# Kernel tuning notes

Hardware: AMD Instinct MI355X
Metric: run time of the kernel (lower is better)

Reference implementation:

```python
import jax, jax.numpy as jnp
import numpy as np


def _decode(out, anchors, t, case, thresh):
    # out: [B, 3*D, H, W] -> [B, H, W, 3, D]; D = 5 + n_classes
    B, C, H, W = out.shape
    o = jnp.transpose(out, (0, 2, 3, 1)).reshape(B, H, W, 3, C // 3)
    mask = o[..., 0] > thresh  # objectness logit threshold (pre-sigmoid, as in original)
    dt = out.dtype
    gx = jnp.arange(W, dtype=dt)  # grid x runs along W (index[:,2] in original)
    gy = jnp.arange(H, dtype=dt)  # grid y runs along H (index[:,1] in original)
    scale = t / case
    cx = (gx[None, None, :, None] + o[..., 1]) * scale
    cy = (gy[None, :, None, None] + o[..., 2]) * scale
    w = anchors[None, None, None, :, 0] * jnp.exp(o[..., 3]) / case
    h = anchors[None, None, None, :, 1] * jnp.exp(o[..., 4]) / case
    p = jax.nn.sigmoid(o[..., 0])
    cls_idx = jnp.argmax(o[..., 5:], axis=-1).astype(dt)
    boxes = jnp.stack([p, cx, cy, w, h, cls_idx], axis=-1).reshape(-1, 6)
    return boxes, mask.reshape(-1)


def setup_inputs() -> dict:
    key = jax.random.key(0)
    k13, k26, k52, kt = jax.random.split(key, 4)
    B = 32
    inp = {
        "output_13": jax.random.normal(k13, (B, 255, 13, 13), dtype=jnp.float32),
        "output_26": jax.random.normal(k26, (B, 255, 26, 26), dtype=jnp.float32),
        "output_52": jax.random.normal(k52, (B, 255, 52, 52), dtype=jnp.float32),
        # canonical YOLOv3 pixel anchors per scale
        "anchors_13": jnp.array([[116.0, 90.0], [156.0, 198.0], [373.0, 326.0]], dtype=jnp.float32),
        "anchors_26": jnp.array([[30.0, 61.0], [62.0, 45.0], [59.0, 119.0]], dtype=jnp.float32),
        "anchors_52": jnp.array([[10.0, 13.0], [16.0, 30.0], [33.0, 23.0]], dtype=jnp.float32),
        "thresh": jnp.array([0.5], dtype=jnp.float32),
        "case": 416,
    }
    return inp


def reference(output_13, output_26, output_52, anchors_13, anchors_26, anchors_52, thresh, case):
    th = thresh[0]
    b13, m13 = _decode(output_13, anchors_13, 32.0, case, th)
    b26, m26 = _decode(output_26, anchors_26, 16.0, case, th)
    b52, m52 = _decode(output_52, anchors_52, 8.0, case, th)
    boxes = jnp.concatenate([b13, b26, b52], axis=0)  # [N_total, 6], row-major (b,h,w,a) per scale
    mask = jnp.concatenate([m13, m26, m52], axis=0)   # boxes[mask] == original torch.cat output
    return boxes, mask
```

## Files before the change

kernel.cpp:

```cpp
#include <hip/hip_runtime.h>


#define NCLS 80

template<int HW, int W>
__device__ __forceinline__ void decode4(
    const float* __restrict__ in, const float* __restrict__ anch,
    float scale, float inv_case, float th,
    int a, int t, int row_base, int B,
    float* __restrict__ boxes, float* __restrict__ mask)
{
    if (t >= B * HW * 4) return;
    const int rt  = t >> 2;
    const int seg = t & 3;
    const int b   = rt / HW;
    const int hw  = rt - b * HW;

    const float* p = in + ((size_t)b * 255 + (size_t)a * 85) * HW + hw;

    const float* pc = p + (size_t)(5 + seg * 20) * HW;
    float v[20];
#pragma unroll
    for (int j = 0; j < 20; ++j)
        v[j] = pc[(size_t)j * HW];

    float best = v[0];
    int   bi   = seg * 20;
#pragma unroll
    for (int j = 1; j < 20; ++j)
        if (v[j] > best) { best = v[j]; bi = seg * 20 + j; }

    float o0 = p[0 * (size_t)HW];
    float o1 = p[1 * (size_t)HW];
    float o2 = p[2 * (size_t)HW];
    float o3 = p[3 * (size_t)HW];
    float o4 = p[4 * (size_t)HW];

#pragma unroll
    for (int m = 1; m <= 2; m <<= 1) {
        float ob = __shfl_xor(best, m);
        int   oi = __shfl_xor(bi,   m);
        if (ob > best || (ob == best && oi < bi)) { best = ob; bi = oi; }
    }

    if (seg == 0) {
        int h = hw / W;
        int w = hw - h * W;
        float px = 1.0f / (1.0f + __expf(-o0));
        float cx = ((float)w + o1) * scale;
        float cy = ((float)h + o2) * scale;
        float bw = anch[2 * a + 0] * __expf(o3) * inv_case;
        float bh = anch[2 * a + 1] * __expf(o4) * inv_case;

        int row = row_base + rt * 3 + a;
        float2* ob2 = reinterpret_cast<float2*>(boxes + (size_t)row * 6);
        ob2[0] = make_float2(px, cx);
        ob2[1] = make_float2(cy, bw);
        ob2[2] = make_float2(bh, (float)bi);
        mask[row] = (o0 > th) ? 1.0f : 0.0f;
    }
}

__global__ __launch_bounds__(256) void detector_kernel(
    const float* __restrict__ in13, const float* __restrict__ in26,
    const float* __restrict__ in52,
    const float* __restrict__ a13, const float* __restrict__ a26,
    const float* __restrict__ a52,
    const float* __restrict__ thp, const int* __restrict__ casep,
    float* __restrict__ boxes, float* __restrict__ mask,
    int B, int nb52, int nb26)
{
    const int a  = blockIdx.y;
    const int bx = blockIdx.x;
    const float th       = thp[0];
    const float inv_case = 1.0f / (float)casep[0];

    if (bx < nb52) {
        int t = bx * 256 + threadIdx.x;
        decode4<2704, 52>(in52, a52, 8.0f * inv_case, inv_case, th,
                          a, t, B * (169 + 676) * 3, B, boxes, mask);
    } else if (bx < nb52 + nb26) {
        int t = (bx - nb52) * 256 + threadIdx.x;
        decode4<676, 26>(in26, a26, 16.0f * inv_case, inv_case, th,
                         a, t, B * 169 * 3, B, boxes, mask);
    } else {
        int t = (bx - nb52 - nb26) * 256 + threadIdx.x;
        decode4<169, 13>(in13, a13, 32.0f * inv_case, inv_case, th,
                         a, t, 0, B, boxes, mask);
    }
}

extern "C" void kernel_launch(void* const* d_in, const int* in_sizes, int n_in,
                              void* d_out, int out_size, void* d_ws, size_t ws_size,
                              hipStream_t stream) {
    const float* in13 = (const float*)d_in[0];
    const float* in26 = (const float*)d_in[1];
    const float* in52 = (const float*)d_in[2];
    const float* a13  = (const float*)d_in[3];
    const float* a26  = (const float*)d_in[4];
    const float* a52  = (const float*)d_in[5];
    const float* thp  = (const float*)d_in[6];
    const int*   casep = (const int*)d_in[7];

    const int B = in_sizes[0] / (255 * 169);

    const int nb52 = (B * 2704 * 4 + 255) / 256;
    const int nb26 = (B * 676  * 4 + 255) / 256;
    const int nb13 = (B * 169  * 4 + 255) / 256;

    const int nrows = B * (169 + 676 + 2704) * 3;
    float* boxes = (float*)d_out;
    float* mask  = (float*)d_out + (size_t)nrows * 6;

    dim3 grid(nb52 + nb26 + nb13, 3);
    detector_kernel<<<grid, 256, 0, stream>>>(
        in13, in26, in52, a13, a26, a52, thp, casep,
        boxes, mask, B, nb52, nb26);
}
```

Baseline: 169.6 us.

## Stage channel tiles into LDS with async double-buffered global_load_lds

Each block now handles one (batch, anchor, spatial tile) and streams all 85 channels into LDS in 8 phases of 11 channels. It uses the global_load_lds builtin with 16-byte transfers where alignment allows, and double-buffers so the next phase loads while the current one is reduced. Each thread owns one or more cells and computes the full argmax itself, which removes the 4-way split and the cross-lane shuffles. The aim is deeper memory-level parallelism and wider loads. The cost is a large LDS footprint (about 59KB per block), a much smaller grid, hand-coded vmcnt waits and barriers that depend on exact load counts, and redundant overlapping tail loads.

Result: no change. 171.6 us (+1.2%).

```diff
diff --git a/kernel.cpp b/kernel.cpp
--- a/kernel.cpp
+++ b/kernel.cpp
@@ -1,63 +1,137 @@
 #include <hip/hip_runtime.h>
 
 
-#define NCLS 80
+#define PHCH 11
+#define NPH  8
+#define TLMAX 676
 
-template<int HW, int W>
-__device__ __forceinline__ void decode4(
+typedef __attribute__((address_space(1))) const void gv_t;
+typedef __attribute__((address_space(3))) void lv_t;
+
+template<int BYTES>
+__device__ __forceinline__ void gl(const float* g, float* l) {
+    if constexpr (BYTES == 16)
+        __builtin_amdgcn_global_load_lds((gv_t*)g, (lv_t*)l, 16, 0, 0);
+    else
+        __builtin_amdgcn_global_load_lds((gv_t*)g, (lv_t*)l, 4, 0, 0);
+}
+
+__device__ __forceinline__ int nch_wave(int wv, int p) {
+    const int nc = (p == NPH - 1) ? (85 - PHCH * (NPH - 1)) : PHCH;
+    const int n  = nc - wv * 3;
+    return n < 0 ? 0 : (n > 3 ? 3 : n);
+}
+
+__device__ __forceinline__ void waitcnt_vm(int n) {
+    switch (n) {
+        case 0:  asm volatile("s_waitcnt vmcnt(0)" ::: "memory"); break;
+        case 6:  asm volatile("s_waitcnt vmcnt(6)" ::: "memory"); break;
+        default: asm volatile("s_waitcnt vmcnt(9)" ::: "memory"); break;
+    }
+}
+
+template<int HW, int TL, int VF>
+__device__ __forceinline__ int stage(const float* __restrict__ base, float* buf,
+                                     int wv, int lane, int p) {
+    const int c0 = wv * 3;
+    const int n  = nch_wave(wv, p);
+    constexpr int VB = VF * 4;
+    for (int i = 0; i < n; ++i) {
+        const float* g = base + (size_t)(PHCH * p + c0 + i) * HW;
+        float* l = buf + (c0 + i) * TL;
+        gl<VB>(g + (size_t)lane * VF,                  l);
+        gl<VB>(g + 64 * VF + (size_t)lane * VF,        l + 64 * VF);
+        gl<VB>(g + (TL - 64 * VF) + (size_t)lane * VF, l + (TL - 64 * VF));
+    }
+    return 3 * n;
+}
+
+template<int HW, int W, int TILES, int VF>
+__device__ __forceinline__ void decode_staged(
     const float* __restrict__ in, const float* __restrict__ anch,
     float scale, float inv_case, float th,
-    int a, int t, int row_base, int B,
-    float* __restrict__ boxes, float* __restrict__ mask)
+    int u, int B, int row_base,
+    float* __restrict__ boxes, float* __restrict__ mask, float* lds)
 {
-    if (t >= B * HW * 4) return;
-    const int rt  = t >> 2;
-    const int seg = t & 3;
-    const int b   = rt / HW;
-    const int hw  = rt - b * HW;
+    constexpr int TL = HW / TILES;
+    constexpr int SLOTS = (TL + 255) / 256;
 
-    const float* p = in + ((size_t)b * 255 + (size_t)a * 85) * HW + hw;
+    const int tile = u % TILES;
+    const int a    = (u / TILES) % 3;
+    const int b    = u / (TILES * 3);
+    const int tid  = threadIdx.x;
+    const int wv   = tid >> 6;
+    const int lane = tid & 63;
 
-    const float* pc = p + (size_t)(5 + seg * 20) * HW;
-    float v[20];
+    const float* base = in + ((size_t)b * 255 + (size_t)a * 85) * HW + (size_t)tile * TL;
+
+    stage<HW, TL, VF>(base, lds, wv, lane, 0);
+
+    float best[SLOTS];
+    int   bi[SLOTS];
+    float bx[5][SLOTS];
 #pragma unroll
-    for (int j = 0; j < 20; ++j)
-        v[j] = pc[(size_t)j * HW];
+    for (int s = 0; s < SLOTS; ++s) { best[s] = -1e30f; bi[s] = 0; }
 
-    float best = v[0];
-    int   bi   = seg * 20;
+    for (int p = 0; p < NPH; ++p) {
+        float* buf = lds + (p & 1) * (PHCH * TL);
+        int wcnt = 0;
+        if (p + 1 < NPH)
+            wcnt = stage<HW, TL, VF>(base, lds + ((p + 1) & 1) * (PHCH * TL), wv, lane, p + 1);
+        waitcnt_vm(wcnt);
+        __builtin_amdgcn_s_barrier();
+        asm volatile("" ::: "memory");
+
+        if (p == 0) {
 #pragma unroll
-    for (int j = 1; j < 20; ++j)
-        if (v[j] > best) { best = v[j]; bi = seg * 20 + j; }
-
-    float o0 = p[0 * (size_t)HW];
-    float o1 = p[1 * (size_t)HW];
-    float o2 = p[2 * (size_t)HW];
-    float o3 = p[3 * (size_t)HW];
-    float o4 = p[4 * (size_t)HW];
-
+            for (int cl = 0; cl < PHCH; ++cl) {
 #pragma unroll
-    for (int m = 1; m <= 2; m <<= 1) {
-        float ob = __shfl_xor(best, m);
-        int   oi = __shfl_xor(bi,   m);
-        if (ob > best || (ob == best && oi < bi)) { best = ob; bi = oi; }
+                for (int s = 0; s < SLOTS; ++s) {
+                    const int hw = tid + s * 256;
+                    if ((s + 1) * 256 <= TL || hw < TL) {
+                        const float v = buf[cl * TL + hw];
+                        if (cl < 5) bx[cl][s] = v;
+                        else if (v > best[s]) { best[s] = v; bi[s] = cl - 5; }
+                    }
+                }
+            }
+        } else {
+            const int nc = (p == NPH - 1) ? (85 - PHCH * (NPH - 1)) : PHCH;
+            for (int cl = 0; cl < nc; ++cl) {
+#pragma unroll
+                for (int s = 0; s < SLOTS; ++s) {
+                    const int hw = tid + s * 256;
+                    if ((s + 1) * 256 <= TL || hw < TL) {
+                        const float v = buf[cl * TL + hw];
+                        if (v > best[s]) { best[s] = v; bi[s] = p * PHCH + cl - 5; }
+                    }
+                }
+            }
+        }
+        asm volatile("" ::: "memory");
+        __builtin_amdgcn_s_barrier();
     }
 
-    if (seg == 0) {
-        int h = hw / W;
-        int w = hw - h * W;
-        float px = 1.0f / (1.0f + __expf(-o0));
-        float cx = ((float)w + o1) * scale;
-        float cy = ((float)h + o2) * scale;
-        float bw = anch[2 * a + 0] * __expf(o3) * inv_case;
-        float bh = anch[2 * a + 1] * __expf(o4) * inv_case;
-
-        int row = row_base + rt * 3 + a;
-        float2* ob2 = reinterpret_cast<float2*>(boxes + (size_t)row * 6);
-        ob2[0] = make_float2(px, cx);
-        ob2[1] = make_float2(cy, bw);
-        ob2[2] = make_float2(bh, (float)bi);
-        mask[row] = (o0 > th) ? 1.0f : 0.0f;
+    const float a0 = anch[2 * a + 0], a1 = anch[2 * a + 1];
+#pragma unroll
+    for (int s = 0; s < SLOTS; ++s) {
+        const int hwl = tid + s * 256;
+        if ((s + 1) * 256 <= TL || hwl < TL) {
+            const int ghw = tile * TL + hwl;
+            const int hh = ghw / W;
+            const int ww = ghw - hh * W;
+            const float px = 1.0f / (1.0f + __expf(-bx[0][s]));
+            const float cx = ((float)ww + bx[1][s]) * scale;
+            const float cy = ((float)hh + bx[2][s]) * scale;
+            const float bw = a0 * __expf(bx[3][s]) * inv_case;
+            const float bh = a1 * __expf(bx[4][s]) * inv_case;
+            const int row = row_base + (b * HW + ghw) * 3 + a;
+            float2* ob2 = reinterpret_cast<float2*>(boxes + (size_t)row * 6);
+            ob2[0] = make_float2(px, cx);
+            ob2[1] = make_float2(cy, bw);
+            ob2[2] = make_float2(bh, (float)bi[s]);
+            mask[row] = (bx[0][s] > th) ? 1.0f : 0.0f;
+        }
     }
 }
 
@@ -67,27 +141,24 @@
     const float* __restrict__ a13, const float* __restrict__ a26,
     const float* __restrict__ a52,
     const float* __restrict__ thp, const int* __restrict__ casep,
-    float* __restrict__ boxes, float* __restrict__ mask,
-    int B, int nb52, int nb26)
+    float* __restrict__ boxes, float* __restrict__ mask, int B)
 {
-    const int a  = blockIdx.y;
-    const int bx = blockIdx.x;
+    __shared__ float lds[2 * PHCH * TLMAX];
+    const int gx = blockIdx.x;
     const float th       = thp[0];
     const float inv_case = 1.0f / (float)casep[0];
+    const int n52 = B * 12;
+    const int n26 = B * 3;
 
-    if (bx < nb52) {
-        int t = bx * 256 + threadIdx.x;
-        decode4<2704, 52>(in52, a52, 8.0f * inv_case, inv_case, th,
-                          a, t, B * (169 + 676) * 3, B, boxes, mask);
-    } else if (bx < nb52 + nb26) {
-        int t = (bx - nb52) * 256 + threadIdx.x;
-        decode4<676, 26>(in26, a26, 16.0f * inv_case, inv_case, th,
-                         a, t, B * 169 * 3, B, boxes, mask);
-    } else {
-        int t = (bx - nb52 - nb26) * 256 + threadIdx.x;
-        decode4<169, 13>(in13, a13, 32.0f * inv_case, inv_case, th,
-                         a, t, 0, B, boxes, mask);
-    }
+    if (gx < n52)
+        decode_staged<2704, 52, 4, 4>(in52, a52, 8.0f * inv_case, inv_case, th,
+                                      gx, B, B * (169 + 676) * 3, boxes, mask, lds);
+    else if (gx < n52 + n26)
+        decode_staged<676, 26, 1, 4>(in26, a26, 16.0f * inv_case, inv_case, th,
+                                     gx - n52, B, B * 169 * 3, boxes, mask, lds);
+    else
+        decode_staged<169, 13, 1, 1>(in13, a13, 32.0f * inv_case, inv_case, th,
+                                     gx - n52 - n26, B, 0, boxes, mask, lds);
 }
 
 extern "C" void kernel_launch(void* const* d_in, const int* in_sizes, int n_in,
@@ -104,16 +175,11 @@
 
     const int B = in_sizes[0] / (255 * 169);
 
-    const int nb52 = (B * 2704 * 4 + 255) / 256;
-    const int nb26 = (B * 676  * 4 + 255) / 256;
-    const int nb13 = (B * 169  * 4 + 255) / 256;
-
     const int nrows = B * (169 + 676 + 2704) * 3;
     float* boxes = (float*)d_out;
     float* mask  = (float*)d_out + (size_t)nrows * 6;
 
-    dim3 grid(nb52 + nb26 + nb13, 3);
+    dim3 grid(B * 18);
     detector_kernel<<<grid, 256, 0, stream>>>(
-        in13, in26, in52, a13, a26, a52, thp, casep,
-        boxes, mask, B, nb52, nb26);
+        in13, in26, in52, a13, a26, a52, thp, casep, boxes, mask, B);
 }
```

## Restructure decode to one block per (batch, anchor) with float4 streaming argmax

Applied to the files above, without the earlier changes.

Replaces the old mapping, where four threads split a cell's 80 classes and combined results with shuffles. Now each block handles one (batch, anchor) plane, and each thread walks all 80 class channels sequentially using float4 loads over four adjacent cells, with a software-prefetched next channel. The goal is wider coalesced loads and no cross-lane reductions. The cost is a grid shrunk to B*9 blocks with heavy per-thread serial work, which may reduce parallelism and memory-level concurrency. Tie-breaking still keeps the first maximum.

Result: slower. 200.3 us (+18.1%).

```diff
diff --git a/kernel.cpp b/kernel.cpp
--- a/kernel.cpp
+++ b/kernel.cpp
@@ -1,64 +1,135 @@
 #include <hip/hip_runtime.h>
 
 
-#define NCLS 80
+__device__ __forceinline__ void upd4(float4& best, float4& bidx,
+                                     const float4 v, const float ci) {
+    if (v.x > best.x) { best.x = v.x; bidx.x = ci; }
+    if (v.y > best.y) { best.y = v.y; bidx.y = ci; }
+    if (v.z > best.z) { best.z = v.z; bidx.z = ci; }
+    if (v.w > best.w) { best.w = v.w; bidx.w = ci; }
+}
 
-template<int HW, int W>
-__device__ __forceinline__ void decode4(
+__device__ __forceinline__ float comp(const float4& v, int k) {
+    switch (k) { case 0: return v.x; case 1: return v.y;
+                 case 2: return v.z; default: return v.w; }
+}
+
+template<int HW, int W, int SLOTS>
+__device__ __forceinline__ void decode_stream4(
     const float* __restrict__ in, const float* __restrict__ anch,
     float scale, float inv_case, float th,
-    int a, int t, int row_base, int B,
+    int b, int a, int row_base,
     float* __restrict__ boxes, float* __restrict__ mask)
 {
-    if (t >= B * HW * 4) return;
-    const int rt  = t >> 2;
-    const int seg = t & 3;
-    const int b   = rt / HW;
-    const int hw  = rt - b * HW;
+    constexpr int HW4 = HW / 4;
+    const int t = threadIdx.x;
+    if (SLOTS == 1 && t >= HW4) return;
 
-    const float* p = in + ((size_t)b * 255 + (size_t)a * 85) * HW + hw;
+    const float4* __restrict__ base =
+        reinterpret_cast<const float4*>(in) + ((size_t)b * 255 + (size_t)a * 85) * HW4;
 
-    const float* pc = p + (size_t)(5 + seg * 20) * HW;
-    float v[20];
+    auto act = [&](int s) { return (s + 1) * 256 <= HW4 ? true : (s * 256 + t < HW4); };
+
+    float4 best[SLOTS], bidx[SLOTS];
 #pragma unroll
-    for (int j = 0; j < 20; ++j)
-        v[j] = pc[(size_t)j * HW];
-
-    float best = v[0];
-    int   bi   = seg * 20;
-#pragma unroll
-    for (int j = 1; j < 20; ++j)
-        if (v[j] > best) { best = v[j]; bi = seg * 20 + j; }
-
-    float o0 = p[0 * (size_t)HW];
-    float o1 = p[1 * (size_t)HW];
-    float o2 = p[2 * (size_t)HW];
-    float o3 = p[3 * (size_t)HW];
-    float o4 = p[4 * (size_t)HW];
-
-#pragma unroll
-    for (int m = 1; m <= 2; m <<= 1) {
-        float ob = __shfl_xor(best, m);
-        int   oi = __shfl_xor(bi,   m);
-        if (ob > best || (ob == best && oi < bi)) { best = ob; bi = oi; }
+    for (int s = 0; s < SLOTS; ++s) {
+        best[s] = make_float4(-1e30f, -1e30f, -1e30f, -1e30f);
+        bidx[s] = make_float4(0.f, 0.f, 0.f, 0.f);
     }
 
-    if (seg == 0) {
-        int h = hw / W;
-        int w = hw - h * W;
-        float px = 1.0f / (1.0f + __expf(-o0));
-        float cx = ((float)w + o1) * scale;
-        float cy = ((float)h + o2) * scale;
-        float bw = anch[2 * a + 0] * __expf(o3) * inv_case;
-        float bh = anch[2 * a + 1] * __expf(o4) * inv_case;
+    float4 cur[SLOTS], nxt[SLOTS];
+#pragma unroll
+    for (int s = 0; s < SLOTS; ++s)
+        if (act(s)) cur[s] = base[(size_t)5 * HW4 + s * 256 + t];
 
-        int row = row_base + rt * 3 + a;
-        float2* ob2 = reinterpret_cast<float2*>(boxes + (size_t)row * 6);
-        ob2[0] = make_float2(px, cx);
-        ob2[1] = make_float2(cy, bw);
-        ob2[2] = make_float2(bh, (float)bi);
-        mask[row] = (o0 > th) ? 1.0f : 0.0f;
+#pragma unroll 2
+    for (int c = 5; c < 84; ++c) {
+#pragma unroll
+        for (int s = 0; s < SLOTS; ++s)
+            if (act(s)) nxt[s] = base[(size_t)(c + 1) * HW4 + s * 256 + t];
+        const float ci = (float)(c - 5);
+#pragma unroll
+        for (int s = 0; s < SLOTS; ++s)
+            upd4(best[s], bidx[s], cur[s], ci);
+#pragma unroll
+        for (int s = 0; s < SLOTS; ++s)
+            cur[s] = nxt[s];
     }
+#pragma unroll
+    for (int s = 0; s < SLOTS; ++s)
+        upd4(best[s], bidx[s], cur[s], 79.f);
+
+    const float a0 = anch[2 * a + 0], a1 = anch[2 * a + 1];
+#pragma unroll
+    for (int s = 0; s < SLOTS; ++s) {
+        if (!act(s)) continue;
+        float4 bx0 = base[(size_t)0 * HW4 + s * 256 + t];
+        float4 bx1 = base[(size_t)1 * HW4 + s * 256 + t];
+        float4 bx2 = base[(size_t)2 * HW4 + s * 256 + t];
+        float4 bx3 = base[(size_t)3 * HW4 + s * 256 + t];
+        float4 bx4 = base[(size_t)4 * HW4 + s * 256 + t];
+#pragma unroll
+        for (int k = 0; k < 4; ++k) {
+            const int hw = (s * 256 + t) * 4 + k;
+            const int hh = hw / W;
+            const int ww = hw - hh * W;
+            const float e0 = comp(bx0, k);
+            const float px = 1.f / (1.f + __expf(-e0));
+            const float cx = ((float)ww + comp(bx1, k)) * scale;
+            const float cy = ((float)hh + comp(bx2, k)) * scale;
+            const float bw = a0 * __expf(comp(bx3, k)) * inv_case;
+            const float bh = a1 * __expf(comp(bx4, k)) * inv_case;
+            const int row = row_base + (b * HW + hw) * 3 + a;
+            float2* ob2 = reinterpret_cast<float2*>(boxes + (size_t)row * 6);
+            ob2[0] = make_float2(px, cx);
+            ob2[1] = make_float2(cy, bw);
+            ob2[2] = make_float2(bh, comp(bidx[s], k));
+            mask[row] = (e0 > th) ? 1.0f : 0.0f;
+        }
+    }
+}
+
+__device__ __forceinline__ void decode_stream13(
+    const float* __restrict__ in, const float* __restrict__ anch,
+    float scale, float inv_case, float th,
+    int b, int a, int row_base,
+    float* __restrict__ boxes, float* __restrict__ mask)
+{
+    constexpr int HW = 169, W = 13;
+    const int t = threadIdx.x;
+    if (t >= HW) return;
+
+    const float* __restrict__ base = in + ((size_t)b * 255 + (size_t)a * 85) * HW + t;
+
+    float best = -1e30f, bidx = 0.f;
+    float cur = base[(size_t)5 * HW], nxt;
+#pragma unroll 2
+    for (int c = 5; c < 84; ++c) {
+        nxt = base[(size_t)(c + 1) * HW];
+        if (cur > best) { best = cur; bidx = (float)(c - 5); }
+        cur = nxt;
+    }
+    if (cur > best) { best = cur; bidx = 79.f; }
+
+    const float e0 = base[0 * (size_t)HW];
+    const float o1 = base[1 * (size_t)HW];
+    const float o2 = base[2 * (size_t)HW];
+    const float o3 = base[3 * (size_t)HW];
+    const float o4 = base[4 * (size_t)HW];
+
+    const int hh = t / W;
+    const int ww = t - hh * W;
+    const float px = 1.f / (1.f + __expf(-e0));
+    const float cx = ((float)ww + o1) * scale;
+    const float cy = ((float)hh + o2) * scale;
+    const float bw = anch[2 * a + 0] * __expf(o3) * inv_case;
+    const float bh = anch[2 * a + 1] * __expf(o4) * inv_case;
+    const int row = row_base + (b * HW + t) * 3 + a;
+    float2* ob2 = reinterpret_cast<float2*>(boxes + (size_t)row * 6);
+    ob2[0] = make_float2(px, cx);
+    ob2[1] = make_float2(cy, bw);
+    ob2[2] = make_float2(bh, bidx);
+    mask[row] = (e0 > th) ? 1.0f : 0.0f;
 }
 
 __global__ __launch_bounds__(256) void detector_kernel(
@@ -67,26 +138,27 @@
     const float* __restrict__ a13, const float* __restrict__ a26,
     const float* __restrict__ a52,
     const float* __restrict__ thp, const int* __restrict__ casep,
-    float* __restrict__ boxes, float* __restrict__ mask,
-    int B, int nb52, int nb26)
+    float* __restrict__ boxes, float* __restrict__ mask, int B)
 {
-    const int a  = blockIdx.y;
-    const int bx = blockIdx.x;
+    const int gx = blockIdx.x;
     const float th       = thp[0];
     const float inv_case = 1.0f / (float)casep[0];
+    const int n52 = B * 3;
 
-    if (bx < nb52) {
-        int t = bx * 256 + threadIdx.x;
-        decode4<2704, 52>(in52, a52, 8.0f * inv_case, inv_case, th,
-                          a, t, B * (169 + 676) * 3, B, boxes, mask);
-    } else if (bx < nb52 + nb26) {
-        int t = (bx - nb52) * 256 + threadIdx.x;
-        decode4<676, 26>(in26, a26, 16.0f * inv_case, inv_case, th,
-                         a, t, B * 169 * 3, B, boxes, mask);
+    if (gx < n52) {
+        const int b = gx / 3, a = gx - b * 3;
+        decode_stream4<2704, 52, 3>(in52, a52, 8.0f * inv_case, inv_case, th,
+                                    b, a, B * (169 + 676) * 3, boxes, mask);
+    } else if (gx < 2 * n52) {
+        const int u = gx - n52;
+        const int b = u / 3, a = u - b * 3;
+        decode_stream4<676, 26, 1>(in26, a26, 16.0f * inv_case, inv_case, th,
+                                   b, a, B * 169 * 3, boxes, mask);
     } else {
-        int t = (bx - nb52 - nb26) * 256 + threadIdx.x;
-        decode4<169, 13>(in13, a13, 32.0f * inv_case, inv_case, th,
-                         a, t, 0, B, boxes, mask);
+        const int u = gx - 2 * n52;
+        const int b = u / 3, a = u - b * 3;
+        decode_stream13(in13, a13, 32.0f * inv_case, inv_case, th,
+                        b, a, 0, boxes, mask);
     }
 }
 
@@ -104,16 +176,11 @@
 
     const int B = in_sizes[0] / (255 * 169);
 
-    const int nb52 = (B * 2704 * 4 + 255) / 256;
-    const int nb26 = (B * 676  * 4 + 255) / 256;
-    const int nb13 = (B * 169  * 4 + 255) / 256;
-
     const int nrows = B * (169 + 676 + 2704) * 3;
     float* boxes = (float*)d_out;
     float* mask  = (float*)d_out + (size_t)nrows * 6;
 
-    dim3 grid(nb52 + nb26 + nb13, 3);
+    dim3 grid(B * 9);
     detector_kernel<<<grid, 256, 0, stream>>>(
-        in13, in26, in52, a13, a26, a52, thp, casep,
-        boxes, mask, B, nb52, nb26);
+        in13, in26, in52, a13, a26, a52, thp, casep, boxes, mask, B);
 }
```

## Vectorize 52/26 scale decode with float4 nontemporal loads and two-way class split

Applied to the files above, without the earlier changes.

For the 52 and 26 scales, each thread now reads four adjacent spatial positions as a float4 with nontemporal loads. The 80 classes are split across two half-waves of 40 classes each, and the two halves are combined with a single cross-lane shuffle. The grid becomes one-dimensional, and the 13 scale keeps the old scalar path with nontemporal loads added. The aim is fewer, wider memory transactions and less cache pollution for this bandwidth-bound read of about 200 MB. The cost is that each thread does more serial work and writes four scattered box rows.

Measured after the change: 169.5 us. About the same (-0.0%).

```diff
diff --git a/kernel.cpp b/kernel.cpp
--- a/kernel.cpp
+++ b/kernel.cpp
@@ -1,7 +1,88 @@
 #include <hip/hip_runtime.h>
 
 
-#define NCLS 80
+typedef float vf4 __attribute__((ext_vector_type(4)));
+
+__device__ __forceinline__ float4 ntld4(const float4* p) {
+    const vf4 v = __builtin_nontemporal_load(reinterpret_cast<const vf4*>(p));
+    return make_float4(v.x, v.y, v.z, v.w);
+}
+
+template<int HW4, int W>
+__device__ __forceinline__ void decode_stream2(
+    const float* __restrict__ in, const float* __restrict__ anch,
+    float scale, float inv_case, float th,
+    int col, int seg, int ncols, int row_base,
+    float* __restrict__ boxes, float* __restrict__ mask)
+{
+    constexpr int HW = HW4 * 4;
+    if (col >= ncols) return;
+    const int slice = col / HW4;
+    const int hw4   = col - slice * HW4;
+    const int b     = slice / 3;
+    const int a     = slice - b * 3;
+
+    const float4* s4 = reinterpret_cast<const float4*>(in)
+                     + (size_t)slice * 85 * HW4 + hw4;
+    const float4* cp = s4 + (size_t)(5 + seg * 40) * HW4;
+
+    float4 best = make_float4(-1e30f, -1e30f, -1e30f, -1e30f);
+    int4   bidx = make_int4(0, 0, 0, 0);
+#pragma unroll 8
+    for (int j = 0; j < 40; ++j) {
+        const float4 v = ntld4(&cp[(size_t)j * HW4]);
+        if (v.x > best.x) { best.x = v.x; bidx.x = j; }
+        if (v.y > best.y) { best.y = v.y; bidx.y = j; }
+        if (v.z > best.z) { best.z = v.z; bidx.z = j; }
+        if (v.w > best.w) { best.w = v.w; bidx.w = j; }
+    }
+    const int g = seg * 40;
+    bidx.x += g; bidx.y += g; bidx.z += g; bidx.w += g;
+
+    {
+        float ob; int oi;
+        ob = __shfl_xor(best.x, 32); oi = __shfl_xor(bidx.x, 32);
+        if (ob > best.x || (ob == best.x && oi < bidx.x)) { best.x = ob; bidx.x = oi; }
+        ob = __shfl_xor(best.y, 32); oi = __shfl_xor(bidx.y, 32);
+        if (ob > best.y || (ob == best.y && oi < bidx.y)) { best.y = ob; bidx.y = oi; }
+        ob = __shfl_xor(best.z, 32); oi = __shfl_xor(bidx.z, 32);
+        if (ob > best.z || (ob == best.z && oi < bidx.z)) { best.z = ob; bidx.z = oi; }
+        ob = __shfl_xor(best.w, 32); oi = __shfl_xor(bidx.w, 32);
+        if (ob > best.w || (ob == best.w && oi < bidx.w)) { best.w = ob; bidx.w = oi; }
+    }
+    if (seg) return;
+
+    const float4 o0 = ntld4(&s4[0]);
+    const float4 o1 = ntld4(&s4[(size_t)1 * HW4]);
+    const float4 o2 = ntld4(&s4[(size_t)2 * HW4]);
+    const float4 o3 = ntld4(&s4[(size_t)3 * HW4]);
+    const float4 o4 = ntld4(&s4[(size_t)4 * HW4]);
+    const float a0 = anch[2 * a + 0], a1 = anch[2 * a + 1];
+
+    const float e0[4] = { o0.x, o0.y, o0.z, o0.w };
+    const float e1[4] = { o1.x, o1.y, o1.z, o1.w };
+    const float e2[4] = { o2.x, o2.y, o2.z, o2.w };
+    const float e3[4] = { o3.x, o3.y, o3.z, o3.w };
+    const float e4[4] = { o4.x, o4.y, o4.z, o4.w };
+    const int   bi[4] = { bidx.x, bidx.y, bidx.z, bidx.w };
+#pragma unroll
+    for (int k = 0; k < 4; ++k) {
+        const int hw = hw4 * 4 + k;
+        const int hh = hw / W;
+        const int ww = hw - hh * W;
+        const float px = 1.f / (1.f + __expf(-e0[k]));
+        const float cx = ((float)ww + e1[k]) * scale;
+        const float cy = ((float)hh + e2[k]) * scale;
+        const float bw = a0 * __expf(e3[k]) * inv_case;
+        const float bh = a1 * __expf(e4[k]) * inv_case;
+        const int row = row_base + (b * HW + hw) * 3 + a;
+        float2* ob2 = reinterpret_cast<float2*>(boxes + (size_t)row * 6);
+        ob2[0] = make_float2(px, cx);
+        ob2[1] = make_float2(cy, bw);
+        ob2[2] = make_float2(bh, (float)bi[k]);
+        mask[row] = (e0[k] > th) ? 1.0f : 0.0f;
+    }
+}
 
 template<int HW, int W>
 __device__ __forceinline__ void decode4(
@@ -22,7 +103,7 @@
     float v[20];
 #pragma unroll
     for (int j = 0; j < 20; ++j)
-        v[j] = pc[(size_t)j * HW];
+        v[j] = __builtin_nontemporal_load(&pc[(size_t)j * HW]);
 
     float best = v[0];
     int   bi   = seg * 20;
@@ -68,23 +149,29 @@
     const float* __restrict__ a52,
     const float* __restrict__ thp, const int* __restrict__ casep,
     float* __restrict__ boxes, float* __restrict__ mask,
-    int B, int nb52, int nb26)
+    int B, int nwg52, int nwg26, int nb13)
 {
-    const int a  = blockIdx.y;
-    const int bx = blockIdx.x;
+    const int gx   = blockIdx.x;
+    const int tid  = threadIdx.x;
+    const int wv   = tid >> 6;
+    const int lane = tid & 63;
     const float th       = thp[0];
     const float inv_case = 1.0f / (float)casep[0];
 
-    if (bx < nb52) {
-        int t = bx * 256 + threadIdx.x;
-        decode4<2704, 52>(in52, a52, 8.0f * inv_case, inv_case, th,
-                          a, t, B * (169 + 676) * 3, B, boxes, mask);
-    } else if (bx < nb52 + nb26) {
-        int t = (bx - nb52) * 256 + threadIdx.x;
-        decode4<676, 26>(in26, a26, 16.0f * inv_case, inv_case, th,
-                         a, t, B * 169 * 3, B, boxes, mask);
+    if (gx < nwg52) {
+        const int col = gx * 128 + wv * 32 + (lane & 31);
+        decode_stream2<676, 52>(in52, a52, 8.0f * inv_case, inv_case, th,
+                                col, lane >> 5, B * 3 * 676,
+                                B * (169 + 676) * 3, boxes, mask);
+    } else if (gx < nwg52 + nwg26) {
+        const int col = (gx - nwg52) * 128 + wv * 32 + (lane & 31);
+        decode_stream2<169, 26>(in26, a26, 16.0f * inv_case, inv_case, th,
+                                col, lane >> 5, B * 3 * 169,
+                                B * 169 * 3, boxes, mask);
     } else {
-        int t = (bx - nb52 - nb26) * 256 + threadIdx.x;
+        const int u = gx - nwg52 - nwg26;
+        const int a = u / nb13;
+        const int t = (u - a * nb13) * 256 + tid;
         decode4<169, 13>(in13, a13, 32.0f * inv_case, inv_case, th,
                          a, t, 0, B, boxes, mask);
     }
@@ -104,16 +191,16 @@
 
     const int B = in_sizes[0] / (255 * 169);
 
-    const int nb52 = (B * 2704 * 4 + 255) / 256;
-    const int nb26 = (B * 676  * 4 + 255) / 256;
-    const int nb13 = (B * 169  * 4 + 255) / 256;
+    const int nwg52 = (B * 3 * 676 + 127) / 128;
+    const int nwg26 = (B * 3 * 169 + 127) / 128;
+    const int nb13  = (B * 169 * 4 + 255) / 256;
 
     const int nrows = B * (169 + 676 + 2704) * 3;
     float* boxes = (float*)d_out;
     float* mask  = (float*)d_out + (size_t)nrows * 6;
 
-    dim3 grid(nb52 + nb26 + nb13, 3);
+    dim3 grid(nwg52 + nwg26 + 3 * nb13);
     detector_kernel<<<grid, 256, 0, stream>>>(
         in13, in26, in52, a13, a26, a52, thp, casep,
-        boxes, mask, B, nb52, nb26);
-}
+        boxes, mask, B, nwg52, nwg26, nb13);
+}
```
